# Kernel optimization log

Measured on AMD Instinct MI355X. Metric: run time of the kernel, lower is better.

The kernel has to match this reference:

```python
import jax, jax.numpy as jnp
import numpy as np

WS = 8           # window size
NUM_HEADS = 16
DIM = 512
HEAD_DIM = DIM // NUM_HEADS


def _relative_position_index(ws):
    coords = np.stack(np.meshgrid(np.arange(ws), np.arange(ws), indexing='ij'))  # (2, ws, ws)
    cf = coords.reshape(2, -1)                                   # (2, ws*ws)
    rel = cf[:, :, None] - cf[:, None, :]                        # (2, N, N)
    rel = rel.transpose(1, 2, 0).copy()
    rel[:, :, 0] += ws - 1
    rel[:, :, 1] += ws - 1
    rel[:, :, 0] *= 2 * ws - 1
    return jnp.asarray(rel.sum(-1))                              # (N, N) int


REL_IDX = _relative_position_index(WS)


def setup_inputs() -> dict:
    key = jax.random.key(0)
    ks = jax.random.split(key, 4)
    B, C, H, W = 4, DIM, 128, 128
    x = jax.random.normal(ks[0], (B, C, H, W), dtype=jnp.float32)
    gamma = jnp.ones((DIM,), jnp.float32)
    beta = jnp.zeros((DIM,), jnp.float32)
    w_qkv = jax.random.normal(ks[1], (DIM, 3 * DIM), jnp.float32) * (DIM ** -0.5)
    w_proj = jax.random.normal(ks[2], (DIM, DIM), jnp.float32) * (DIM ** -0.5)
    b_proj = jnp.zeros((DIM,), jnp.float32)
    bias_table = jax.random.normal(ks[3], ((2 * WS - 1) ** 2, NUM_HEADS), jnp.float32) * 0.02
    return {"x": x, "gamma": gamma, "beta": beta, "w_qkv": w_qkv,
            "w_proj": w_proj, "b_proj": b_proj, "bias_table": bias_table}


def reference(x, gamma, beta, w_qkv, w_proj, b_proj, bias_table):
    B, C, H, W = x.shape
    pad_h = (WS - H % WS) % WS
    pad_w = (WS - W % WS) % WS
    x = jnp.pad(x, ((0, 0), (0, 0), (0, pad_h), (0, pad_w)))
    Hp, Wp = H + pad_h, W + pad_w
    nh, nw = Hp // WS, Wp // WS
    N = WS * WS  # tokens per window

    # window partition: (B,C,Hp,Wp) -> (B*nh*nw, N, C)
    xw = x.reshape(B, C, nh, WS, nw, WS).transpose(0, 2, 4, 3, 5, 1)
    xw = xw.reshape(B * nh * nw, N, C)

    # LayerNorm over channels
    mu = jnp.mean(xw, axis=-1, keepdims=True)
    var = jnp.var(xw, axis=-1, keepdims=True)
    xn = (xw - mu) * jax.lax.rsqrt(var + 1e-5) * gamma + beta

    # QKV projection (no bias)
    qkv = (xn @ w_qkv).reshape(-1, N, 3, NUM_HEADS, HEAD_DIM)
    qkv = qkv.transpose(2, 0, 3, 1, 4)   # (3, nWin, heads, N, hd)
    q, k, v = qkv[0], qkv[1], qkv[2]

    scale = HEAD_DIM ** -0.5
    attn = jnp.einsum('whnd,whmd->whnm', q, k) * scale          # (nWin, heads, N, N)
    rel_bias = bias_table[REL_IDX]                               # (N, N, heads)
    attn = attn + rel_bias.transpose(2, 0, 1)[None]
    attn = jax.nn.softmax(attn, axis=-1)

    out = jnp.einsum('whnm,whmd->wnhd', attn, v).reshape(-1, N, C)
    out = out @ w_proj + b_proj

    # un-window: (B*nh*nw, N, C) -> (B, C, Hp, Wp)
    out = out.reshape(B, nh, nw, WS, WS, C).transpose(0, 5, 1, 3, 2, 4)
    out = out.reshape(B, C, Hp, Wp)
    return out[:, :, :H, :W]
```

## Files before the change

### kernel.cpp

```cpp
#include <hip/hip_runtime.h>

typedef unsigned short u16;
typedef unsigned int u32;
typedef __bf16 bf16x8 __attribute__((ext_vector_type(8)));
typedef float f32x4 __attribute__((ext_vector_type(4)));

#define C_DIM 512
#define QKV_N 1536
#define KDIM 512
#define NHEAD 16
#define HD 32
#define H_IMG 128
#define W_IMG 128
#define HW 16384
#define NTOK 65536
#define NWIN 1024

#define GLL(g, l) __builtin_amdgcn_global_load_lds( \
    (const __attribute__((address_space(1))) u32*)(g), \
    (__attribute__((address_space(3))) u32*)(l), 16, 0, 0)

#define BAR() __builtin_amdgcn_s_barrier()
#define LGKM0() asm volatile("s_waitcnt lgkmcnt(0)" ::: "memory")
#define VM6() asm volatile("s_waitcnt vmcnt(6)" ::: "memory")
#define VM0() asm volatile("s_waitcnt vmcnt(0)" ::: "memory")

__device__ __forceinline__ u16 f2bf(float f) {
    u32 u = __builtin_bit_cast(u32, f);
    u += 0x7fffu + ((u >> 16) & 1u);
    return (u16)(u >> 16);
}
__device__ __forceinline__ float bf2f(u16 v) {
    return __builtin_bit_cast(float, (u32)v << 16);
}

__global__ void sa_prep_kernel(const float* __restrict__ w_qkv,
                               const float* __restrict__ w_proj,
                               const float* __restrict__ bias_table,
                               u16* __restrict__ wqT, u16* __restrict__ wpT,
                               u16* __restrict__ biasP) {
    int t = blockIdx.x * 256 + threadIdx.x;
    const int W1 = KDIM * QKV_N;
    const int W2 = KDIM * C_DIM;
    const int W3 = NHEAD * 64 * 64;
    if (t < W1) {
        int k = t / QKV_N, n = t % QKV_N;
        wqT[n * KDIM + k] = f2bf(w_qkv[t]);
    } else if (t < W1 + W2) {
        int u = t - W1;
        int k = u / C_DIM, n = u % C_DIM;
        wpT[n * KDIM + k] = f2bf(w_proj[u]);
    } else if (t < W1 + W2 + W3) {
        int u = t - W1 - W2;
        int h = u >> 12, n = (u >> 6) & 63, m = u & 63;
        int di = (n >> 3) - (m >> 3) + 7;
        int dj = (n & 7) - (m & 7) + 7;
        biasP[u] = f2bf(bias_table[(di * 15 + dj) * NHEAD + h]);
    }
}

__global__ __launch_bounds__(512, 4) void sa_ln_fused_kernel(const float* __restrict__ x,
        const float* __restrict__ gamma, const float* __restrict__ beta,
        u16* __restrict__ xnc) {
    __shared__ u16 tile[64 * 513];
    __shared__ float ssum[8][64], ssq[8][64];
    __shared__ float smu[64], srs[64];
    int bid = blockIdx.x;
    int win = (bid & 7) * (NWIN / 8) + (bid >> 3);
    int b = win >> 8, wl = win & 255;
    int wh = wl >> 4, ww = wl & 15;
    int tid = threadIdx.x;
    int n = tid & 63;
    int gq = tid >> 6;
    int s_n = (wh * 8 + (n >> 3)) * W_IMG + ww * 8 + (n & 7);
    const float* xb = x + (size_t)b * C_DIM * HW + s_n;
    float sum = 0.f, sq = 0.f;
#pragma unroll 8
    for (int it = 0; it < 64; ++it) {
        int c = it * 8 + gq;
        float v = xb[(size_t)c * HW];
        _Float16 hv = (_Float16)v;
        tile[n * 513 + c] = __builtin_bit_cast(u16, hv);
        sum += v; sq += v * v;
    }
    ssum[gq][n] = sum; ssq[gq][n] = sq;
    __syncthreads();
    if (tid < 64) {
        float S = 0.f, Q = 0.f;
#pragma unroll
        for (int k = 0; k < 8; ++k) { S += ssum[k][n]; Q += ssq[k][n]; }
        float m = S * (1.f / C_DIM);
        float var = Q * (1.f / C_DIM) - m * m;
        smu[n] = m; srs[n] = rsqrtf(var + 1e-5f);
    }
    __syncthreads();
    float gg[8], bb[8];
#pragma unroll
    for (int c0 = 0; c0 < 8; ++c0) { gg[c0] = gamma[c0 * 64 + n]; bb[c0] = beta[c0 * 64 + n]; }
#pragma unroll
    for (int it = 0; it < 8; ++it) {
        int nn = it * 8 + gq;
        float m = smu[nn], r = srs[nn];
        u16* op = xnc + (size_t)((win << 6) + nn) * C_DIM;
#pragma unroll
        for (int c0 = 0; c0 < 8; ++c0) {
            int c = c0 * 64 + n;
            float v = (float)__builtin_bit_cast(_Float16, tile[nn * 513 + c]);
            op[c] = f2bf((v - m) * r * gg[c0] + bb[c0]);
        }
    }
}


#define LDA1(Q,J,KK,BUF) af[Q][J][KK] = *reinterpret_cast<const bf16x8*>( \
    &lds[(BUF)*16384 + (wr*128 + ((Q)*2+(J))*16 + lr)*64 + ((((KK)*4)+lg) ^ (lr & 7))*8])
#define LDAQ(Q,BUF) do{ LDA1(Q,0,0,BUF); LDA1(Q,0,1,BUF); LDA1(Q,1,0,BUF); LDA1(Q,1,1,BUF); }while(0)
#define LDB1(NF,KK,BUF) bfr[NF][KK] = *reinterpret_cast<const bf16x8*>( \
    &lds[32768 + (BUF)*16384 + (wc*64 + (NF)*16 + lr)*64 + ((((KK)*4)+lg) ^ (lr & 7))*8])
#define LDB(BUF) do{ LDB1(0,0,BUF); LDB1(0,1,BUF); LDB1(1,0,BUF); LDB1(1,1,BUF); \
                     LDB1(2,0,BUF); LDB1(2,1,BUF); LDB1(3,0,BUF); LDB1(3,1,BUF); }while(0)
#define MFMA1(M,N,KK) acc[M][N] = __builtin_amdgcn_mfma_f32_16x16x32_bf16(af[(M)/2][(M)&1][KK], bfr[N][KK], acc[M][N], 0, 0, 0)
#define MFMAQ(Q) do{ __builtin_amdgcn_s_setprio(1); \
    MFMA1(2*(Q),0,0);   MFMA1(2*(Q),0,1);   MFMA1(2*(Q),1,0);   MFMA1(2*(Q),1,1); \
    MFMA1(2*(Q),2,0);   MFMA1(2*(Q),2,1);   MFMA1(2*(Q),3,0);   MFMA1(2*(Q),3,1); \
    MFMA1(2*(Q)+1,0,0); MFMA1(2*(Q)+1,0,1); MFMA1(2*(Q)+1,1,0); MFMA1(2*(Q)+1,1,1); \
    MFMA1(2*(Q)+1,2,0); MFMA1(2*(Q)+1,2,1); MFMA1(2*(Q)+1,3,0); MFMA1(2*(Q)+1,3,1); \
    __builtin_amdgcn_s_setprio(0); }while(0)
#define STAGE_A(SRC, KT, H) do{ const u16* _s = (SRC) + (KT)*64 + (size_t)((H)*128)*KDIM; \
    u16* _d = Adst + ((KT)&1)*16384 + (H)*8192; \
    GLL(_s, _d); GLL(_s + (size_t)64*KDIM, _d + 4096); }while(0)
#define STAGE_B(SRC, KT, H) do{ const u16* _s = (SRC) + (KT)*64 + (size_t)((H)*128)*KDIM; \
    u16* _d = Bdst + ((KT)&1)*16384 + (H)*8192; \
    GLL(_s, _d); GLL(_s + (size_t)64*KDIM, _d + 4096); }while(0)

template <int EPI>
__device__ __forceinline__ void gemm8_body(const u16* __restrict__ A,
        const u16* __restrict__ BT, u16* __restrict__ outB, float* __restrict__ outF,
        const float* __restrict__ bias, int nbx, int NT, u16* lds, int nblk) {
    const int tid = threadIdx.x;
    const int lane = tid & 63, wv = tid >> 6;
    const int wr = wv >> 2, wc = wv & 3;
    const int lr = lane & 15, lg = lane >> 4;
    const int arow = tid >> 3;
    const int axs = ((tid & 7) ^ ((tid >> 3) & 7)) * 8;
    u16* Adst = lds + tid * 8;
    u16* Bdst = lds + 32768 + tid * 8;

    const int cpx = nblk >> 3;
    const int t = ((int)blockIdx.x & 7) * cpx + ((int)blockIdx.x >> 3);
    const int mb = t / nbx, nb = t % nbx;
    const int m0 = mb * 256, n0 = nb * 256;
    const u16* Asrc = A  + (size_t)(m0 + arow) * KDIM + axs;
    const u16* Bsrc = BT + (size_t)(n0 + arow) * KDIM + axs;

    bf16x8 af[4][2][2];
    bf16x8 bfr[4][2];

    STAGE_A(Asrc, 0, 0); STAGE_A(Asrc, 0, 1); STAGE_B(Bsrc, 0, 0); STAGE_B(Bsrc, 0, 1);
    STAGE_B(Bsrc, 1, 0); STAGE_B(Bsrc, 1, 1); STAGE_A(Asrc, 1, 0);
    VM6(); BAR();

    f32x4 acc[8][4];
#pragma unroll
    for (int i = 0; i < 8; ++i)
#pragma unroll
        for (int j = 0; j < 4; ++j) acc[i][j] = {0.f, 0.f, 0.f, 0.f};

#pragma unroll 1
    for (int i = 0; i < 3; ++i) {
        LDB(0); LDAQ(0, 0); STAGE_A(Asrc, 2*i + 1, 1);
        BAR(); LGKM0(); MFMAQ(0); BAR();
        LDAQ(1, 0); LDAQ(2, 0); STAGE_B(Bsrc, 2*i + 2, 0);
        BAR(); LGKM0(); MFMAQ(1); BAR();
        LDAQ(3, 0); STAGE_B(Bsrc, 2*i + 2, 1);
        BAR(); LGKM0(); MFMAQ(2); BAR();
        STAGE_A(Asrc, 2*i + 2, 0);
        BAR(); LGKM0(); MFMAQ(3); VM6(); BAR();
        LDB(1); LDAQ(0, 1); STAGE_A(Asrc, 2*i + 2, 1);
        BAR(); LGKM0(); MFMAQ(0); BAR();
        LDAQ(1, 1); LDAQ(2, 1); STAGE_B(Bsrc, 2*i + 3, 0);
        BAR(); LGKM0(); MFMAQ(1); BAR();
        LDAQ(3, 1); STAGE_B(Bsrc, 2*i + 3, 1);
        BAR(); LGKM0(); MFMAQ(2); BAR();
        STAGE_A(Asrc, 2*i + 3, 0);
        BAR(); LGKM0(); MFMAQ(3); VM6(); BAR();
    }
    LDB(0); LDAQ(0, 0); STAGE_A(Asrc, 7, 1);
    BAR(); LGKM0(); MFMAQ(0); BAR();
    LDAQ(1, 0); LDAQ(2, 0);
    BAR(); LGKM0(); MFMAQ(1); BAR();
    LDAQ(3, 0);
    BAR(); LGKM0(); MFMAQ(2); BAR();
    BAR(); LGKM0(); MFMAQ(3); VM0(); BAR();
    LDB(1); LDAQ(0, 1);
    BAR(); LGKM0(); MFMAQ(0); BAR();
    LDAQ(1, 1); LDAQ(2, 1);
    BAR(); LGKM0(); MFMAQ(1); BAR();
    LDAQ(3, 1);
    BAR(); LGKM0(); MFMAQ(2); BAR();
    BAR(); LGKM0(); MFMAQ(3);

    if (EPI == 0) {
#pragma unroll
        for (int mf = 0; mf < 8; ++mf) {
#pragma unroll
            for (int nf = 0; nf < 4; ++nf) {
                int col = n0 + wc * 64 + nf * 16 + lr;
                int row = m0 + wr * 128 + mf * 16 + lg * 4;
#pragma unroll
                for (int rr = 0; rr < 4; ++rr)
                    outB[(size_t)(row + rr) * NT + col] = f2bf(acc[mf][nf][rr]);
            }
        }
    } else {
        int win0 = m0 >> 6;
        int b_img = win0 >> 8, wl = win0 & 255;
        int h0 = (wl >> 4) * 8, w0 = (wl & 15) * 8;
        float* fbuf = reinterpret_cast<float*>(lds);
        __syncthreads();
#pragma unroll
        for (int s = 0; s < 2; ++s) {
            if ((wc >> 1) == s) {
                int half = wc & 1;
                float* cb = fbuf + half * 16384;
#pragma unroll
                for (int mf = 0; mf < 8; ++mf) {
#pragma unroll
                    for (int nf = 0; nf < 4; ++nf) {
                        int cp = nf * 16 + lr;
                        int row = wr * 128 + mf * 16 + lg * 4;
                        int h = (row >> 3) & 7;
                        int sl = ((row >> 6) & 3) * 2 + ((row >> 2) & 1);
                        float bbv = bias[n0 + (2 * s + half) * 64 + cp];
                        f32x4 v = acc[mf][nf];
                        float4 o = {v[0] + bbv, v[1] + bbv, v[2] + bbv, v[3] + bbv};
                        *reinterpret_cast<float4*>(&cb[cp * 256 + h * 32 + (sl ^ (cp & 7)) * 4]) = o;
                    }
                }
            }
            __syncthreads();
#pragma unroll
            for (int j = 0; j < 16; ++j) {
                int flat = j * 512 + tid;
                int half = flat >> 12, f = flat & 4095;
                int cp = f >> 6, h = (f >> 3) & 7, sl = f & 7;
                int col = n0 + (2 * s + half) * 64 + cp;
                float4 v = *reinterpret_cast<const float4*>(
                    &fbuf[half * 16384 + cp * 256 + h * 32 + ((sl ^ (cp & 7))) * 4]);
                *reinterpret_cast<float4*>(outF + (size_t)(b_img * C_DIM + col) * HW
                                           + (size_t)(h0 + h) * W_IMG + w0 + sl * 4) = v;
            }
            __syncthreads();
        }
    }
}

__global__ __launch_bounds__(512, 2) void sa_qkv_gemm(const u16* __restrict__ A,
        const u16* __restrict__ BT, u16* __restrict__ outB) {
    __shared__ u16 lds[65536];
    gemm8_body<0>(A, BT, outB, nullptr, nullptr, 6, QKV_N, lds, 1536);
}

__global__ __launch_bounds__(512, 2) void sa_proj_gemm(const u16* __restrict__ A,
        const u16* __restrict__ BT, float* __restrict__ outF, const float* __restrict__ bias) {
    __shared__ u16 lds[65536];
    gemm8_body<1>(A, BT, nullptr, outF, bias, 2, C_DIM, lds, 512);
}

__global__ __launch_bounds__(64) void sa_attn_kernel(const u16* __restrict__ qkv,
        const u16* __restrict__ biasP, u16* __restrict__ attnc) {
    __shared__ u16 Ps[64 * 72];
    int bid = blockIdx.x;
    int win  = (bid & 7) * 128 + (bid >> 7);
    int head = (bid >> 3) & 15;
    int lane = threadIdx.x, lr = lane & 15, lg = lane >> 4;
    const u16* base = qkv + (size_t)win * 64 * QKV_N + head * HD;

    bf16x8 qa[4], kb[4];
#pragma unroll
    for (int mt = 0; mt < 4; ++mt)
        qa[mt] = *reinterpret_cast<const bf16x8*>(base + (size_t)(mt * 16 + lr) * QKV_N + lg * 8);
#pragma unroll
    for (int nt = 0; nt < 4; ++nt)
        kb[nt] = *reinterpret_cast<const bf16x8*>(base + (size_t)(nt * 16 + lr) * QKV_N + 512 + lg * 8);

    f32x4 sacc[4][4];
#pragma unroll
    for (int i = 0; i < 4; ++i)
#pragma unroll
        for (int j = 0; j < 4; ++j) sacc[i][j] = {0.f, 0.f, 0.f, 0.f};
#pragma unroll
    for (int mt = 0; mt < 4; ++mt)
#pragma unroll
        for (int nt = 0; nt < 4; ++nt)
            sacc[mt][nt] = __builtin_amdgcn_mfma_f32_16x16x32_bf16(qa[mt], kb[nt], sacc[mt][nt], 0, 0, 0);

    union { u16 s[8]; bf16x8 v; } vb[2][2];
#pragma unroll
    for (int ks = 0; ks < 2; ++ks)
#pragma unroll
        for (int n2 = 0; n2 < 2; ++n2)
#pragma unroll
            for (int i = 0; i < 8; ++i)
                vb[ks][n2].s[i] = base[(size_t)(ks * 32 + lg * 8 + i) * QKV_N + 1024 + n2 * 16 + lr];

    const float scale = 0.17677669529663687f;
    const u16* bp = biasP + head * 4096;
#pragma unroll
    for (int mt = 0; mt < 4; ++mt) {
#pragma unroll
        for (int rr = 0; rr < 4; ++rr) {
            int row = mt * 16 + lg * 4 + rr;
            float vals[4];
#pragma unroll
            for (int nt = 0; nt < 4; ++nt)
                vals[nt] = sacc[mt][nt][rr] * scale + bf2f(bp[row * 64 + nt * 16 + lr]);
            float mx = fmaxf(fmaxf(vals[0], vals[1]), fmaxf(vals[2], vals[3]));
#pragma unroll
            for (int d = 1; d < 16; d <<= 1) mx = fmaxf(mx, __shfl_xor(mx, d, 64));
            float sm = 0.f;
#pragma unroll
            for (int nt = 0; nt < 4; ++nt) { vals[nt] = __expf(vals[nt] - mx); sm += vals[nt]; }
#pragma unroll
            for (int d = 1; d < 16; d <<= 1) sm += __shfl_xor(sm, d, 64);
            float inv = 1.f / sm;
#pragma unroll
            for (int nt = 0; nt < 4; ++nt)
                Ps[row * 72 + nt * 16 + lr] = f2bf(vals[nt] * inv);
        }
    }
    __syncthreads();

    f32x4 oacc[4][2];
#pragma unroll
    for (int i = 0; i < 4; ++i) { oacc[i][0] = {0.f,0.f,0.f,0.f}; oacc[i][1] = {0.f,0.f,0.f,0.f}; }
#pragma unroll
    for (int ks = 0; ks < 2; ++ks) {
        bf16x8 pa[4];
#pragma unroll
        for (int mt = 0; mt < 4; ++mt)
            pa[mt] = *reinterpret_cast<const bf16x8*>(&Ps[(mt * 16 + lr) * 72 + ks * 32 + lg * 8]);
#pragma unroll
        for (int mt = 0; mt < 4; ++mt)
#pragma unroll
            for (int n2 = 0; n2 < 2; ++n2)
                oacc[mt][n2] = __builtin_amdgcn_mfma_f32_16x16x32_bf16(pa[mt], vb[ks][n2].v, oacc[mt][n2], 0, 0, 0);
    }

#pragma unroll
    for (int mt = 0; mt < 4; ++mt)
#pragma unroll
        for (int n2 = 0; n2 < 2; ++n2)
#pragma unroll
            for (int rr = 0; rr < 4; ++rr) {
                int row = mt * 16 + lg * 4 + rr;
                attnc[(size_t)(win * 64 + row) * C_DIM + head * HD + n2 * 16 + lr] =
                    f2bf(oacc[mt][n2][rr]);
            }
}

extern "C" void kernel_launch(void* const* d_in, const int* in_sizes, int n_in,
                              void* d_out, int out_size, void* d_ws, size_t ws_size,
                              hipStream_t stream) {
    const float* x          = (const float*)d_in[0];
    const float* gamma      = (const float*)d_in[1];
    const float* beta       = (const float*)d_in[2];
    const float* w_qkv      = (const float*)d_in[3];
    const float* w_proj     = (const float*)d_in[4];
    const float* b_proj     = (const float*)d_in[5];
    const float* bias_table = (const float*)d_in[6];
    float* out = (float*)d_out;

    char* ws = (char*)d_ws;
    size_t off = 0;
    auto alloc = [&](size_t bytes) {
        char* p = ws + off;
        off += (bytes + 255) & ~(size_t)255;
        return p;
    };
    u16*   wqT   = (u16*)alloc((size_t)KDIM * QKV_N * 2);
    u16*   wpT   = (u16*)alloc((size_t)KDIM * C_DIM * 2);
    u16*   biasP = (u16*)alloc((size_t)NHEAD * 64 * 64 * 2);
    u16*   xnc   = (u16*)alloc((size_t)NTOK * C_DIM * 2);
    u16*   qkvc  = (u16*)alloc((size_t)NTOK * QKV_N * 2);
    u16*   attnc = (u16*)alloc((size_t)NTOK * C_DIM * 2);

    sa_prep_kernel<<<4352, 256, 0, stream>>>(w_qkv, w_proj, bias_table, wqT, wpT, biasP);
    sa_ln_fused_kernel<<<NWIN, 512, 0, stream>>>(x, gamma, beta, xnc);
    sa_qkv_gemm<<<1536, 512, 0, stream>>>(xnc, wqT, qkvc);
    sa_attn_kernel<<<NWIN * NHEAD, 64, 0, stream>>>(qkvc, biasP, attnc);
    sa_proj_gemm<<<512, 512, 0, stream>>>(attnc, wpT, out, b_proj);
}
```

Baseline: 333.5 us.

## Give QKV GEMM its own 256x128 tile kernel with 4 waves and K=32 stages

Splits the QKV projection out of the shared GEMM template into a dedicated kernel using 256-thread blocks, 256x128 output tiles and K-steps of 32 with a smaller double-buffered LDS footprint (48KB vs 128KB). This doubles the grid to 3072 blocks, aiming for better occupancy and load balance across CUs. The trade-off is less reuse per tile (more global A reloads across N tiles) and more barriers per K step. The projection GEMM is specialised in place with hard-coded tile mapping.

```diff
diff --git a/kernel.cpp b/kernel.cpp
--- a/kernel.cpp
+++ b/kernel.cpp
@@ -112,14 +112,88 @@
 }
 
 
-#define LDA1(Q,J,KK,BUF) af[Q][J][KK] = *reinterpret_cast<const bf16x8*>( \
+#define QLDA(MF,BUF) af[MF] = *reinterpret_cast<const bf16x8*>( \
+    &lds[(BUF)*12288 + (wr*128 + (MF)*16 + lr)*32 + (lg ^ ((lr>>1)&3))*8])
+#define QLDB(NF,BUF) bfr[NF] = *reinterpret_cast<const bf16x8*>( \
+    &lds[(BUF)*12288 + 8192 + (wc*64 + (NF)*16 + lr)*32 + (lg ^ ((lr>>1)&3))*8])
+#define QLDB4(BUF) do{ QLDB(0,BUF); QLDB(1,BUF); QLDB(2,BUF); QLDB(3,BUF); }while(0)
+#define QLDA03(BUF) do{ QLDA(0,BUF); QLDA(1,BUF); QLDA(2,BUF); QLDA(3,BUF); }while(0)
+#define QLDA47(BUF) do{ QLDA(4,BUF); QLDA(5,BUF); QLDA(6,BUF); QLDA(7,BUF); }while(0)
+#define QMFMA1(M,N) acc[M][N] = __builtin_amdgcn_mfma_f32_16x16x32_bf16(af[M], bfr[N], acc[M][N], 0, 0, 0)
+#define QMFMA16(M0) do{ __builtin_amdgcn_s_setprio(1); \
+    QMFMA1((M0)+0,0); QMFMA1((M0)+0,1); QMFMA1((M0)+0,2); QMFMA1((M0)+0,3); \
+    QMFMA1((M0)+1,0); QMFMA1((M0)+1,1); QMFMA1((M0)+1,2); QMFMA1((M0)+1,3); \
+    QMFMA1((M0)+2,0); QMFMA1((M0)+2,1); QMFMA1((M0)+2,2); QMFMA1((M0)+2,3); \
+    QMFMA1((M0)+3,0); QMFMA1((M0)+3,1); QMFMA1((M0)+3,2); QMFMA1((M0)+3,3); \
+    __builtin_amdgcn_s_setprio(0); }while(0)
+#define QSTAGE_A(KT) do{ const u16* _s = Aq + (KT)*32; \
+    u16* _d = lds + ((KT)&1)*12288 + tid*8; \
+    GLL(_s, _d);                       GLL(_s + (size_t) 64*KDIM, _d + 2048); \
+    GLL(_s + (size_t)128*KDIM, _d + 4096); GLL(_s + (size_t)192*KDIM, _d + 6144); }while(0)
+#define QSTAGE_B(KT) do{ const u16* _s = Bq + (KT)*32; \
+    u16* _d = lds + ((KT)&1)*12288 + 8192 + tid*8; \
+    GLL(_s, _d); GLL(_s + (size_t)64*KDIM, _d + 2048); }while(0)
+
+__global__ __launch_bounds__(256, 2) void sa_qkv_gemm(const u16* __restrict__ A,
+        const u16* __restrict__ BT, u16* __restrict__ outB) {
+    __shared__ u16 lds[24576];
+
+    const int tid = threadIdx.x;
+    const int lane = tid & 63, wv = tid >> 6;
+    const int wr = wv >> 1, wc = wv & 1;
+    const int lr = lane & 15, lg = lane >> 4;
+    const int axs = ((tid & 3) ^ ((tid >> 3) & 3)) * 8;
+
+    const int t = ((int)blockIdx.x & 7) * 384 + ((int)blockIdx.x >> 3);
+    const int mb = t / 12, nb = t % 12;
+    const int m0 = mb * 256, n0 = nb * 128;
+    const u16* Aq = A  + (size_t)(m0 + (tid >> 2)) * KDIM + axs;
+    const u16* Bq = BT + (size_t)(n0 + (tid >> 2)) * KDIM + axs;
+
+    bf16x8 af[8], bfr[4];
+    f32x4 acc[8][4];
+#pragma unroll
+    for (int i = 0; i < 8; ++i)
+#pragma unroll
+        for (int j = 0; j < 4; ++j) acc[i][j] = {0.f, 0.f, 0.f, 0.f};
+
+    QSTAGE_A(0); QSTAGE_B(0);
+    VM0(); BAR();
+
+#pragma unroll 1
+    for (int i = 0; i < 8; ++i) {
+        QLDB4(0); QLDA03(0); QSTAGE_A(2*i + 1);
+        BAR(); LGKM0(); QMFMA16(0); BAR();
+        QLDA47(0); QSTAGE_B(2*i + 1);
+        BAR(); LGKM0(); QMFMA16(4); VM0(); BAR();
+        QLDB4(1); QLDA03(1); if (i < 7) { QSTAGE_A(2*i + 2); }
+        BAR(); LGKM0(); QMFMA16(0); BAR();
+        QLDA47(1); if (i < 7) { QSTAGE_B(2*i + 2); }
+        BAR(); LGKM0(); QMFMA16(4); VM0(); BAR();
+    }
+
+#pragma unroll
+    for (int mf = 0; mf < 8; ++mf) {
+#pragma unroll
+        for (int nf = 0; nf < 4; ++nf) {
+            int col = n0 + wc * 64 + nf * 16 + lr;
+            int row = m0 + wr * 128 + mf * 16 + lg * 4;
+#pragma unroll
+            for (int rr = 0; rr < 4; ++rr)
+                outB[(size_t)(row + rr) * QKV_N + col] = f2bf(acc[mf][nf][rr]);
+        }
+    }
+}
+
+
+#define LDA1(Q,J,KK,BUF) paf[Q][J][KK] = *reinterpret_cast<const bf16x8*>( \
     &lds[(BUF)*16384 + (wr*128 + ((Q)*2+(J))*16 + lr)*64 + ((((KK)*4)+lg) ^ (lr & 7))*8])
 #define LDAQ(Q,BUF) do{ LDA1(Q,0,0,BUF); LDA1(Q,0,1,BUF); LDA1(Q,1,0,BUF); LDA1(Q,1,1,BUF); }while(0)
-#define LDB1(NF,KK,BUF) bfr[NF][KK] = *reinterpret_cast<const bf16x8*>( \
+#define LDB1(NF,KK,BUF) pbf[NF][KK] = *reinterpret_cast<const bf16x8*>( \
     &lds[32768 + (BUF)*16384 + (wc*64 + (NF)*16 + lr)*64 + ((((KK)*4)+lg) ^ (lr & 7))*8])
 #define LDB(BUF) do{ LDB1(0,0,BUF); LDB1(0,1,BUF); LDB1(1,0,BUF); LDB1(1,1,BUF); \
                      LDB1(2,0,BUF); LDB1(2,1,BUF); LDB1(3,0,BUF); LDB1(3,1,BUF); }while(0)
-#define MFMA1(M,N,KK) acc[M][N] = __builtin_amdgcn_mfma_f32_16x16x32_bf16(af[(M)/2][(M)&1][KK], bfr[N][KK], acc[M][N], 0, 0, 0)
+#define MFMA1(M,N,KK) acc[M][N] = __builtin_amdgcn_mfma_f32_16x16x32_bf16(paf[(M)/2][(M)&1][KK], pbf[N][KK], acc[M][N], 0, 0, 0)
 #define MFMAQ(Q) do{ __builtin_amdgcn_s_setprio(1); \
     MFMA1(2*(Q),0,0);   MFMA1(2*(Q),0,1);   MFMA1(2*(Q),1,0);   MFMA1(2*(Q),1,1); \
     MFMA1(2*(Q),2,0);   MFMA1(2*(Q),2,1);   MFMA1(2*(Q),3,0);   MFMA1(2*(Q),3,1); \
@@ -133,10 +207,10 @@
     u16* _d = Bdst + ((KT)&1)*16384 + (H)*8192; \
     GLL(_s, _d); GLL(_s + (size_t)64*KDIM, _d + 4096); }while(0)
 
-template <int EPI>
-__device__ __forceinline__ void gemm8_body(const u16* __restrict__ A,
-        const u16* __restrict__ BT, u16* __restrict__ outB, float* __restrict__ outF,
-        const float* __restrict__ bias, int nbx, int NT, u16* lds, int nblk) {
+__global__ __launch_bounds__(512, 2) void sa_proj_gemm(const u16* __restrict__ A,
+        const u16* __restrict__ BT, float* __restrict__ outF, const float* __restrict__ bias) {
+    __shared__ u16 lds[65536];
+
     const int tid = threadIdx.x;
     const int lane = tid & 63, wv = tid >> 6;
     const int wr = wv >> 2, wc = wv & 3;
@@ -146,15 +220,14 @@
     u16* Adst = lds + tid * 8;
     u16* Bdst = lds + 32768 + tid * 8;
 
-    const int cpx = nblk >> 3;
-    const int t = ((int)blockIdx.x & 7) * cpx + ((int)blockIdx.x >> 3);
-    const int mb = t / nbx, nb = t % nbx;
+    const int t = ((int)blockIdx.x & 7) * 64 + ((int)blockIdx.x >> 3);
+    const int mb = t >> 1, nb = t & 1;
     const int m0 = mb * 256, n0 = nb * 256;
     const u16* Asrc = A  + (size_t)(m0 + arow) * KDIM + axs;
     const u16* Bsrc = BT + (size_t)(n0 + arow) * KDIM + axs;
 
-    bf16x8 af[4][2][2];
-    bf16x8 bfr[4][2];
+    bf16x8 paf[4][2][2];
+    bf16x8 pbf[4][2];
 
     STAGE_A(Asrc, 0, 0); STAGE_A(Asrc, 0, 1); STAGE_B(Bsrc, 0, 0); STAGE_B(Bsrc, 0, 1);
     STAGE_B(Bsrc, 1, 0); STAGE_B(Bsrc, 1, 1); STAGE_A(Asrc, 1, 0);
@@ -200,19 +273,7 @@
     BAR(); LGKM0(); MFMAQ(2); BAR();
     BAR(); LGKM0(); MFMAQ(3);
 
-    if (EPI == 0) {
-#pragma unroll
-        for (int mf = 0; mf < 8; ++mf) {
-#pragma unroll
-            for (int nf = 0; nf < 4; ++nf) {
-                int col = n0 + wc * 64 + nf * 16 + lr;
-                int row = m0 + wr * 128 + mf * 16 + lg * 4;
-#pragma unroll
-                for (int rr = 0; rr < 4; ++rr)
-                    outB[(size_t)(row + rr) * NT + col] = f2bf(acc[mf][nf][rr]);
-            }
-        }
-    } else {
+    {
         int win0 = m0 >> 6;
         int b_img = win0 >> 8, wl = win0 & 255;
         int h0 = (wl >> 4) * 8, w0 = (wl & 15) * 8;
@@ -255,18 +316,6 @@
     }
 }
 
-__global__ __launch_bounds__(512, 2) void sa_qkv_gemm(const u16* __restrict__ A,
-        const u16* __restrict__ BT, u16* __restrict__ outB) {
-    __shared__ u16 lds[65536];
-    gemm8_body<0>(A, BT, outB, nullptr, nullptr, 6, QKV_N, lds, 1536);
-}
-
-__global__ __launch_bounds__(512, 2) void sa_proj_gemm(const u16* __restrict__ A,
-        const u16* __restrict__ BT, float* __restrict__ outF, const float* __restrict__ bias) {
-    __shared__ u16 lds[65536];
-    gemm8_body<1>(A, BT, nullptr, outF, bias, 2, C_DIM, lds, 512);
-}
-
 __global__ __launch_bounds__(64) void sa_attn_kernel(const u16* __restrict__ qkv,
         const u16* __restrict__ biasP, u16* __restrict__ attnc) {
     __shared__ u16 Ps[64 * 72];
@@ -387,7 +436,7 @@
 
     sa_prep_kernel<<<4352, 256, 0, stream>>>(w_qkv, w_proj, bias_table, wqT, wpT, biasP);
     sa_ln_fused_kernel<<<NWIN, 512, 0, stream>>>(x, gamma, beta, xnc);
-    sa_qkv_gemm<<<1536, 512, 0, stream>>>(xnc, wqT, qkvc);
+    sa_qkv_gemm<<<3072, 256, 0, stream>>>(xnc, wqT, qkvc);
     sa_attn_kernel<<<NWIN * NHEAD, 64, 0, stream>>>(qkvc, biasP, attnc);
     sa_proj_gemm<<<512, 512, 0, stream>>>(attnc, wpT, out, b_proj);
 }
```

New measurement: 337.6 us. About the same (+1.2%).
